# Kernel optimization log

Measured on AMD Instinct MI355X. Metric: run time of the kernel, lower is better.

Reference implementation:

```python
import jax, jax.numpy as jnp
import numpy as np

HIDDEN = 256


def setup_inputs() -> dict:
    key = jax.random.key(0)
    ks = jax.random.split(key, 16)
    bs, T, wv, vocab, inp = 256, 256, 100, 600, 64
    s = 0.05
    lengths = jax.random.randint(ks[2], (bs,), 2, T + 1)
    lengths = lengths.at[0].set(T)  # ensure max(decoder_length) == T-1
    return {
        "encoder_out": jax.random.normal(ks[0], (bs, inp), jnp.float32),
        "encoded_captions": jax.random.normal(ks[1], (bs, T, wv), jnp.float32),
        "w_ih": jax.random.normal(ks[3], (4 * HIDDEN, inp), jnp.float32) * s,
        "w_hh": jax.random.normal(ks[4], (4 * HIDDEN, HIDDEN), jnp.float32) * s,
        "b_ih": jax.random.normal(ks[5], (4 * HIDDEN,), jnp.float32) * s,
        "b_hh": jax.random.normal(ks[6], (4 * HIDDEN,), jnp.float32) * s,
        "W_out": jax.random.normal(ks[7], (vocab, HIDDEN), jnp.float32) * s,
        "b_out": jax.random.normal(ks[8], (vocab,), jnp.float32) * s,
        "W_emb": jax.random.normal(ks[9], (inp, wv), jnp.float32) * s,
        "b_emb": jax.random.normal(ks[10], (inp,), jnp.float32) * s,
        "W_h": jax.random.normal(ks[11], (HIDDEN, inp), jnp.float32) * s,
        "b_h": jax.random.normal(ks[12], (HIDDEN,), jnp.float32) * s,
        "W_c": jax.random.normal(ks[13], (HIDDEN, inp), jnp.float32) * s,
        "b_c": jax.random.normal(ks[14], (HIDDEN,), jnp.float32) * s,
        "caption_lengths": lengths,
    }


def reference(encoder_out, encoded_captions, w_ih, w_hh, b_ih, b_hh,
              W_out, b_out, W_emb, b_emb, W_h, b_h, W_c, b_c,
              caption_lengths):
    # sort by descending caption length (as torch.sort(descending=True))
    sort_idx = jnp.argsort(-caption_lengths)
    lengths = caption_lengths[sort_idx]
    enc = encoder_out[sort_idx]                  # [bs, 64]
    caps = encoded_captions[sort_idx]            # [bs, T, 100]

    h0 = enc @ W_h.T + b_h                       # [bs, H]
    c0 = enc @ W_c.T + b_c                       # [bs, H]
    emb = caps @ W_emb.T + b_emb                 # [bs, T, 64]

    dec_len = lengths - 1                        # [bs]
    steps = caps.shape[1] - 1                    # == max(dec_len) by construction
    xs = jnp.swapaxes(emb[:, :steps], 0, 1)      # [steps, bs, 64]
    ts = jnp.arange(steps)

    def step(carry, inp):
        h, c = carry
        x, t = inp
        gates = x @ w_ih.T + b_ih + h @ w_hh.T + b_hh      # [bs, 4H]
        i, f, g, o = jnp.split(gates, 4, axis=-1)           # torch gate order i,f,g,o
        i = jax.nn.sigmoid(i); f = jax.nn.sigmoid(f)
        g = jnp.tanh(g);       o = jax.nn.sigmoid(o)
        c_new = f * c + i * g
        h_new = o * jnp.tanh(c_new)
        active = (t < dec_len)[:, None]                     # shrinking batch == mask (sorted)
        logits = h_new @ W_out.T + b_out                    # [bs, vocab]
        pred = jnp.where(active, logits, jnp.float32(-1.0))
        h = jnp.where(active, h_new, h)
        c = jnp.where(active, c_new, c)
        return (h, c), pred

    (_, _), preds = jax.lax.scan(step, (h0, c0), (xs, ts))
    predicts = jnp.swapaxes(preds, 0, 1)         # [bs, steps, vocab]
    return predicts, caps, dec_len, sort_idx
```

## Files before the change

### kernel.cpp

```cpp
#include <hip/hip_runtime.h>
#include <hip/hip_fp16.h>

#define BS 256
#define T 256
#define STEPS 255
#define WV 100
#define INP 64
#define H 256
#define G4 1024
#define VOCAB 600
#define VT 38

typedef _Float16 f16x2 __attribute__((ext_vector_type(2)));
typedef _Float16 f16x8 __attribute__((ext_vector_type(8)));
typedef float f32x4 __attribute__((ext_vector_type(4)));

__device__ __forceinline__ float fdot2(unsigned w, unsigned h, float acc) {
#if defined(__has_builtin) && __has_builtin(__builtin_amdgcn_fdot2)
    return __builtin_amdgcn_fdot2(__builtin_bit_cast(f16x2, w),
                                  __builtin_bit_cast(f16x2, h), acc, false);
#else
    __half2 wv = *(const __half2*)&w;
    __half2 hv = *(const __half2*)&h;
    float2 wf = __half22float2(wv), hf = __half22float2(hv);
    return acc + wf.x * hf.x + wf.y * hf.y;
#endif
}

__device__ __forceinline__ float quad_reduce(float x) {
    int a = __builtin_bit_cast(int, x);
    int b = __builtin_amdgcn_update_dpp(0, a, 0xB1, 0xF, 0xF, true);
    float s = x + __builtin_bit_cast(float, b);
    int c = __builtin_bit_cast(int, s);
    int d = __builtin_amdgcn_update_dpp(0, c, 0x4E, 0xF, 0xF, true);
    return s + __builtin_bit_cast(float, d);
}

__device__ __forceinline__ f32x4 mfma16(uint4 a, uint4 b, f32x4 c) {
    return __builtin_amdgcn_mfma_f32_16x16x32_f16(
        __builtin_bit_cast(f16x8, a), __builtin_bit_cast(f16x8, b), c, 0, 0, 0);
}

__global__ void k_sort(const int* __restrict__ lens, int* __restrict__ sidx,
                       int* __restrict__ dlen, float* __restrict__ out_dec,
                       float* __restrict__ out_sidx) {
    __shared__ int L[BS];
    int i = threadIdx.x;
    L[i] = lens[i];
    __syncthreads();
    int li = L[i];
    int r = 0;
    for (int j = 0; j < BS; ++j) {
        int lj = L[j];
        r += (lj > li) || (lj == li && j < i);
    }
    sidx[r] = i;
    dlen[r] = li - 1;
    out_sidx[r] = (float)i;
    out_dec[r]  = (float)(li - 1);
}

__global__ void k_gather(const float* __restrict__ cin, const int* __restrict__ sidx,
                         float* __restrict__ cout) {
    int b = blockIdx.x;
    int src = sidx[b];
    const float4* in  = (const float4*)(cin + (size_t)src * T * WV);
    float4* out       = (float4*)(cout + (size_t)b * T * WV);
    for (int i = threadIdx.x; i < T * WV / 4; i += 256) out[i] = in[i];
}

__global__ void k_wcomb(const float* __restrict__ w_ih, const float* __restrict__ W_emb,
                        float* __restrict__ Wc) {
    int idx = blockIdx.x * 256 + threadIdx.x;
    int r = idx / WV, cc = idx % WV;
    float acc = 0.f;
    for (int k = 0; k < INP; ++k) acc += w_ih[r * INP + k] * W_emb[k * WV + cc];
    Wc[idx] = acc;
}

__global__ void k_bcomb(const float* __restrict__ w_ih, const float* __restrict__ b_ih,
                        const float* __restrict__ b_hh, const float* __restrict__ b_emb,
                        float* __restrict__ bc) {
    int r = blockIdx.x * 256 + threadIdx.x;
    float acc = b_ih[r] + b_hh[r];
    for (int k = 0; k < INP; ++k) acc += w_ih[r * INP + k] * b_emb[k];
    bc[r] = acc;
}

__global__ void k_packw(const float* __restrict__ w_hh, __half2* __restrict__ wR) {
    int idx = blockIdx.x * 256 + threadIdx.x;
    wR[idx] = __floats2half2_rn(w_hh[(size_t)idx * 2], w_hh[(size_t)idx * 2 + 1]);
}

__global__ void k_packwo(const float* __restrict__ Wo, __half* __restrict__ woHi,
                         __half* __restrict__ woLo) {
    int idx = blockIdx.x * 256 + threadIdx.x;
    int fi = idx >> 9;
    int l  = (idx >> 3) & 63;
    int j  = idx & 7;
    int vt = fi >> 3, kt = fi & 7;
    int v = vt * 16 + (l & 15);
    int k = kt * 32 + ((l >> 4) << 3) + j;
    float w = (v < VOCAB) ? Wo[(size_t)v * H + k] : 0.f;
    __half hi = __float2half(w);
    __half lo = __float2half(w - __half2float(hi));
    woHi[idx] = hi;
    woLo[idx] = lo;
}

__global__ void k_inithc(const float* __restrict__ enc, const int* __restrict__ sidx,
                         const float* __restrict__ W_h, const float* __restrict__ b_h,
                         const float* __restrict__ W_c, const float* __restrict__ b_c,
                         float* __restrict__ h_st, float* __restrict__ c_st) {
    int b = blockIdx.x, j = threadIdx.x;
    __shared__ __align__(16) float e[INP];
    int src = sidx[b];
    if (j < INP) e[j] = enc[src * INP + j];
    __syncthreads();
    const float4* e4  = (const float4*)e;
    const float4* wh4 = (const float4*)(W_h + (size_t)j * INP);
    const float4* wc4 = (const float4*)(W_c + (size_t)j * INP);
    float ah = b_h[j], ac = b_c[j];
    #pragma unroll
    for (int k4 = 0; k4 < INP / 4; ++k4) {
        float4 ev = e4[k4];
        float4 wh = wh4[k4];
        float4 wc = wc4[k4];
        ah += ev.x * wh.x + ev.y * wh.y + ev.z * wh.z + ev.w * wh.w;
        ac += ev.x * wc.x + ev.y * wc.y + ev.z * wc.z + ev.w * wc.w;
    }
    h_st[b * H + j] = ah;
    c_st[b * H + j] = ac;
}

__global__ void k_xg(const float* __restrict__ caps, const float* __restrict__ Wc,
                     const float* __restrict__ bc, const int* __restrict__ dlen,
                     float* __restrict__ xg, int t0, int Cc) {
    int b = blockIdx.y;
    int ct0 = blockIdx.x * 16;
    if (t0 + ct0 >= dlen[b]) return;
    __shared__ __align__(16) float4 cs4[16][WV / 4];
    float* cs = (float*)cs4;
    for (int i = threadIdx.x; i < 16 * WV; i += 256) {
        int rr = i / WV, k = i % WV;
        int t = t0 + ct0 + rr;
        cs[rr * WV + k] = (t < T && ct0 + rr < Cc) ? caps[((size_t)b * T + t) * WV + k] : 0.f;
    }
    __syncthreads();
    int nrow = Cc - ct0; if (nrow > 16) nrow = 16;
    for (int rq = 0; rq < 4; ++rq) {
        int r = threadIdx.x + rq * 256;
        float acc[16];
        float bv = bc[r];
        #pragma unroll
        for (int rr = 0; rr < 16; ++rr) acc[rr] = bv;
        const float4* wr = (const float4*)(Wc + (size_t)r * WV);
        for (int k4 = 0; k4 < WV / 4; ++k4) {
            float4 w = wr[k4];
            #pragma unroll
            for (int rr = 0; rr < 16; ++rr) {
                float4 av = cs4[rr][k4];
                acc[rr] += av.x * w.x + av.y * w.y + av.z * w.z + av.w * w.w;
            }
        }
        for (int rr = 0; rr < nrow; ++rr)
            xg[((size_t)b * Cc + ct0 + rr) * G4 + r] = acc[rr];
    }
}

#define LSTM_SMEM (131072 + 4096 + 1152)

__global__ __launch_bounds__(512)
__attribute__((amdgpu_waves_per_eu(2, 2)))
void k_lstm(const __half2* __restrict__ wR,
        const float* __restrict__ xg, const int* __restrict__ dlen,
        float* __restrict__ h_st, float* __restrict__ c_st,
        __half* __restrict__ hck, int t0, int Cc) {
    extern __shared__ __align__(16) char smem[];
    uint4*    wl4  = (uint4*)smem;
    float*    gv   = (float*)(smem + 131072);
    unsigned* hpad = (unsigned*)(smem + 131072 + 4096);
    unsigned* lpad = hpad + 144;
    const uint4* hh4 = (const uint4*)hpad;
    const uint4* hl4 = (const uint4*)lpad;

    int b = blockIdx.x, tid = threadIdx.x;
    int steps_b = dlen[b];
    if (t0 >= steps_b) return;

    int lane = tid & 63;
    int q = lane & 3;
    int Q = tid >> 2;
    int rowbase = Q * 8;
    int gate = __builtin_amdgcn_readfirstlane(tid >> 7);

    const uint4* wR4 = (const uint4*)wR;

    uint4 wreg[6][8];
    #pragma unroll
    for (int j = 0; j < 6; ++j)
        #pragma unroll
        for (int u = 0; u < 8; ++u)
            wreg[j][u] = wR4[(rowbase + j) * 32 + q * 8 + u];
    #pragma unroll
    for (int s = 0; s < 2; ++s)
        #pragma unroll
        for (int u = 0; u < 8; ++u)
            wl4[((u * 2 + s) * 128 + Q) * 4 + q] = wR4[(rowbase + 6 + s) * 32 + q * 8 + u];

    float c = 0.f, hcur = 0.f;
    if (tid < H) {
        hcur = h_st[b * H + tid];
        c    = c_st[b * H + tid];
        __half hh16 = __float2half(hcur);
        __half hl16 = __float2half(hcur - __half2float(hh16));
        int hidx = (tid >> 6) * 72 + (tid & 63);
        ((__half*)hpad)[hidx] = hh16;
        ((__half*)lpad)[hidx] = hl16;
    }
    __syncthreads();

    int tend = t0 + Cc; if (tend > steps_b) tend = steps_b;
    const float* xgp = xg + (size_t)b * Cc * G4;
    __half* hckp = hck + (size_t)b * Cc * H;

    for (int t = t0; t < tend; ++t) {
        float x0 = xgp[rowbase + q];
        float x1 = xgp[rowbase + 4 + q];

        float ah[8], al[8];
        #pragma unroll
        for (int j = 0; j < 8; ++j) { ah[j] = 0.f; al[j] = 0.f; }

        #pragma unroll
        for (int u = 0; u < 8; ++u) {
            uint4 hh = hh4[q * 9 + u];
            uint4 hl = hl4[q * 9 + u];
            #pragma unroll
            for (int j = 0; j < 6; ++j) {
                uint4 w = wreg[j][u];
                ah[j] = fdot2(w.x, hh.x, ah[j]);
                ah[j] = fdot2(w.y, hh.y, ah[j]);
                ah[j] = fdot2(w.z, hh.z, ah[j]);
                ah[j] = fdot2(w.w, hh.w, ah[j]);
                al[j] = fdot2(w.x, hl.x, al[j]);
                al[j] = fdot2(w.y, hl.y, al[j]);
                al[j] = fdot2(w.z, hl.z, al[j]);
                al[j] = fdot2(w.w, hl.w, al[j]);
            }
            uint4 w6 = wl4[((u * 2 + 0) * 128 + Q) * 4 + q];
            uint4 w7 = wl4[((u * 2 + 1) * 128 + Q) * 4 + q];
            ah[6] = fdot2(w6.x, hh.x, ah[6]);
            ah[6] = fdot2(w6.y, hh.y, ah[6]);
            ah[6] = fdot2(w6.z, hh.z, ah[6]);
            ah[6] = fdot2(w6.w, hh.w, ah[6]);
            al[6] = fdot2(w6.x, hl.x, al[6]);
            al[6] = fdot2(w6.y, hl.y, al[6]);
            al[6] = fdot2(w6.z, hl.z, al[6]);
            al[6] = fdot2(w6.w, hl.w, al[6]);
            ah[7] = fdot2(w7.x, hh.x, ah[7]);
            ah[7] = fdot2(w7.y, hh.y, ah[7]);
            ah[7] = fdot2(w7.z, hh.z, ah[7]);
            ah[7] = fdot2(w7.w, hh.w, ah[7]);
            al[7] = fdot2(w7.x, hl.x, al[7]);
            al[7] = fdot2(w7.y, hl.y, al[7]);
            al[7] = fdot2(w7.z, hl.z, al[7]);
            al[7] = fdot2(w7.w, hl.w, al[7]);
        }

        float tt[8];
        #pragma unroll
        for (int j = 0; j < 8; ++j) tt[j] = quad_reduce(ah[j] + al[j]);

        float k0 = (q == 0) ? tt[0] : (q == 1) ? tt[1] : (q == 2) ? tt[2] : tt[3];
        float k1 = (q == 0) ? tt[4] : (q == 1) ? tt[5] : (q == 2) ? tt[6] : tt[7];
        float p0 = k0 + x0;
        float p1 = k1 + x1;
        if (gate == 2) { p0 = tanhf(p0); p1 = tanhf(p1); }
        else {
            p0 = 1.f / (1.f + __expf(-p0));
            p1 = 1.f / (1.f + __expf(-p1));
        }
        gv[rowbase + q]     = p0;
        gv[rowbase + 4 + q] = p1;
        __syncthreads();

        if (tid < H) {
            float iv  = gv[tid];
            float fv  = gv[256 + tid];
            float gvt = gv[512 + tid];
            float ov  = gv[768 + tid];
            c = fv * c + iv * gvt;
            float nh = ov * tanhf(c);
            hcur = nh;
            __half hh16 = __float2half(nh);
            __half hl16 = __float2half(nh - __half2float(hh16));
            hckp[tid] = hh16;
            int hidx = (tid >> 6) * 72 + (tid & 63);
            ((__half*)hpad)[hidx] = hh16;
            ((__half*)lpad)[hidx] = hl16;
        }
        __syncthreads();
        xgp += G4;
        hckp += H;
    }
    if (tid < H) { h_st[b * H + tid] = hcur; c_st[b * H + tid] = c; }
}

__global__ __launch_bounds__(64) void k_logits(const __half* __restrict__ hck,
        const __half* __restrict__ woHi, const __half* __restrict__ woLo,
        const float* __restrict__ bo, const int* __restrict__ dlen,
        float* __restrict__ pred, int t0, int Cc) {
    int b = blockIdx.y;
    int ct0 = blockIdx.x * 32;
    if (ct0 >= Cc) return;
    int steps_b = dlen[b];
    int l = threadIdx.x;
    int lhi = l >> 4, llo = l & 15;

    if (t0 + ct0 >= steps_b) {
        for (int r = 0; r < 32; ++r) {
            int t = t0 + ct0 + r;
            if (r >= Cc - ct0 || t >= STEPS) break;
            float* pr = pred + ((size_t)b * STEPS + t) * VOCAB;
            for (int v = l; v < VOCAB; v += 64) pr[v] = -1.f;
        }
        return;
    }

    uint4 a[2][8];
    #pragma unroll
    for (int m = 0; m < 2; ++m) {
        int rr = ct0 + m * 16 + llo;
        int rc = (rr < Cc) ? rr : (Cc - 1);
        const uint4* rp = (const uint4*)(hck + ((size_t)b * Cc + rc) * H);
        #pragma unroll
        for (int kt = 0; kt < 8; ++kt) a[m][kt] = rp[kt * 4 + lhi];
    }

    const uint4* bh4 = (const uint4*)woHi;
    const uint4* bl4 = (const uint4*)woLo;
    for (int vt = 0; vt < VT; ++vt) {
        int v = vt * 16 + llo;
        float bias = (v < VOCAB) ? bo[v] : 0.f;
        f32x4 acc0 = {bias, bias, bias, bias};
        f32x4 acc1 = acc0;
        #pragma unroll
        for (int kt = 0; kt < 8; ++kt) {
            uint4 bh = bh4[(vt * 8 + kt) * 64 + l];
            acc0 = mfma16(a[0][kt], bh, acc0);
            acc1 = mfma16(a[1][kt], bh, acc1);
        }
        #pragma unroll
        for (int kt = 0; kt < 8; ++kt) {
            uint4 bl = bl4[(vt * 8 + kt) * 64 + l];
            acc0 = mfma16(a[0][kt], bl, acc0);
            acc1 = mfma16(a[1][kt], bl, acc1);
        }
        if (v < VOCAB) {
            #pragma unroll
            for (int m = 0; m < 2; ++m) {
                f32x4 A = m ? acc1 : acc0;
                #pragma unroll
                for (int i = 0; i < 4; ++i) {
                    int r = ct0 + m * 16 + lhi * 4 + i;
                    int t = t0 + r;
                    if (r < Cc && t < STEPS)
                        pred[((size_t)b * STEPS + t) * VOCAB + v] =
                            (t < steps_b) ? A[i] : -1.f;
                }
            }
        }
    }
}

extern "C" void kernel_launch(void* const* d_in, const int* in_sizes, int n_in,
                              void* d_out, int out_size, void* d_ws, size_t ws_size,
                              hipStream_t stream) {
    const float* enc   = (const float*)d_in[0];
    const float* caps  = (const float*)d_in[1];
    const float* w_ih  = (const float*)d_in[2];
    const float* w_hh  = (const float*)d_in[3];
    const float* b_ih  = (const float*)d_in[4];
    const float* b_hh  = (const float*)d_in[5];
    const float* W_out = (const float*)d_in[6];
    const float* b_out = (const float*)d_in[7];
    const float* W_emb = (const float*)d_in[8];
    const float* b_emb = (const float*)d_in[9];
    const float* W_h   = (const float*)d_in[10];
    const float* b_h   = (const float*)d_in[11];
    const float* W_c   = (const float*)d_in[12];
    const float* b_c   = (const float*)d_in[13];
    const int*   lens  = (const int*)d_in[14];

    float* out_pred = (float*)d_out;
    float* out_caps = out_pred + (size_t)BS * STEPS * VOCAB;
    float* out_dec  = out_caps + (size_t)BS * T * WV;
    float* out_sidx = out_dec + BS;

    char* w = (char*)d_ws;
    size_t off = 0;
    auto take = [&](size_t bytes) -> char* {
        char* p = w + off;
        off += (bytes + 255) & ~(size_t)255;
        return p;
    };
    int*     sidx = (int*)take(BS * 4);
    int*     dlen = (int*)take(BS * 4);
    float*   Wc   = (float*)take((size_t)G4 * WV * 4);
    float*   bc   = (float*)take(G4 * 4);
    float*   h_st = (float*)take((size_t)BS * H * 4);
    float*   c_st = (float*)take((size_t)BS * H * 4);
    __half2* wR   = (__half2*)take((size_t)G4 * (H / 2) * 4);
    __half*  woHi = (__half*)take((size_t)VT * 8 * 64 * 8 * 2);
    __half*  woLo = (__half*)take((size_t)VT * 8 * 64 * 8 * 2);

    size_t rem = (ws_size > off) ? (ws_size - off) : 0;
    size_t per_step = (size_t)BS * G4 * 4 + (size_t)BS * H * 2 + 1024;
    int C = (int)(rem / per_step);
    if (C < 1) C = 1;
    if (C > STEPS) C = STEPS;
    float*  xg  = (float*)take((size_t)BS * C * G4 * 4);
    __half* hck = (__half*)take((size_t)BS * C * H * 2);

    (void)hipFuncSetAttribute((const void*)k_lstm,
                              hipFuncAttributeMaxDynamicSharedMemorySize, LSTM_SMEM);

    k_sort<<<1, 256, 0, stream>>>(lens, sidx, dlen, out_dec, out_sidx);
    k_gather<<<BS, 256, 0, stream>>>(caps, sidx, out_caps);
    k_wcomb<<<G4 * WV / 256, 256, 0, stream>>>(w_ih, W_emb, Wc);
    k_bcomb<<<G4 / 256, 256, 0, stream>>>(w_ih, b_ih, b_hh, b_emb, bc);
    k_packw<<<G4 * (H / 2) / 256, 256, 0, stream>>>(w_hh, wR);
    k_packwo<<<VT * 8 * 64 * 8 / 256, 256, 0, stream>>>(W_out, woHi, woLo);
    k_inithc<<<BS, 256, 0, stream>>>(enc, sidx, W_h, b_h, W_c, b_c, h_st, c_st);

    for (int t0 = 0; t0 < STEPS; t0 += C) {
        int Cc = STEPS - t0; if (Cc > C) Cc = C;
        dim3 gx((Cc + 15) / 16, BS);
        dim3 gl((Cc + 31) / 32, BS);
        k_xg<<<gx, 256, 0, stream>>>(out_caps, Wc, bc, dlen, xg, t0, Cc);
        k_lstm<<<BS, 512, LSTM_SMEM, stream>>>(wR, xg, dlen, h_st, c_st, hck, t0, Cc);
        k_logits<<<gl, 64, 0, stream>>>(hck, woHi, woLo, b_out, dlen, out_pred, t0, Cc);
    }
}
```

Measured before the change: 1.504 ms.

## Compute input-gate projection with split-fp16 MFMA instead of scalar FP32

Caption embeddings and the combined input weight are each split into fp16 hi/lo pairs and packed into MFMA fragment layouts. The xg kernel then uses 16x16 MFMA tiles with three products per tile (hi*hi, hi*lo, lo*hi) in place of the FP32 scalar dot-product loop. This targets the FP32 ALU cost of the input projection. It adds two pack kernels and extra workspace for the packed captions, and slightly changes numerics.

```diff
diff --git a/kernel.cpp b/kernel.cpp
--- a/kernel.cpp
+++ b/kernel.cpp
@@ -106,6 +106,32 @@
     __half lo = __float2half(w - __half2float(hi));
     woHi[idx] = hi;
     woLo[idx] = lo;
+}
+
+__global__ void k_packcaps(const float* __restrict__ caps, __half* __restrict__ cHi,
+                           __half* __restrict__ cLo) {
+    int idx = blockIdx.x * 256 + threadIdx.x;
+    int k = idx & 127;
+    int bt = idx >> 7;
+    float v = (k < WV) ? caps[(size_t)bt * WV + k] : 0.f;
+    __half hi = __float2half(v);
+    cHi[idx] = hi;
+    cLo[idx] = __float2half(v - __half2float(hi));
+}
+
+__global__ void k_packwc(const float* __restrict__ Wc, __half* __restrict__ wcHi,
+                         __half* __restrict__ wcLo) {
+    int idx = blockIdx.x * 256 + threadIdx.x;
+    int fi = idx >> 9;
+    int l  = (idx >> 3) & 63;
+    int j  = idx & 7;
+    int nt = fi >> 2, kt = fi & 3;
+    int n = nt * 16 + (l & 15);
+    int k = kt * 32 + ((l >> 4) << 3) + j;
+    float w = (k < WV) ? Wc[(size_t)n * WV + k] : 0.f;
+    __half hi = __float2half(w);
+    wcHi[idx] = hi;
+    wcLo[idx] = __float2half(w - __half2float(hi));
 }
 
 __global__ void k_inithc(const float* __restrict__ enc, const int* __restrict__ sidx,
@@ -133,38 +159,57 @@
     c_st[b * H + j] = ac;
 }
 
-__global__ void k_xg(const float* __restrict__ caps, const float* __restrict__ Wc,
-                     const float* __restrict__ bc, const int* __restrict__ dlen,
-                     float* __restrict__ xg, int t0, int Cc) {
+__global__ __launch_bounds__(256) void k_xg(const __half* __restrict__ cHi,
+        const __half* __restrict__ cLo, const __half* __restrict__ wcHi,
+        const __half* __restrict__ wcLo, const float* __restrict__ bc,
+        const int* __restrict__ dlen, float* __restrict__ xg, int t0, int Cc) {
     int b = blockIdx.y;
-    int ct0 = blockIdx.x * 16;
+    int ct0 = blockIdx.x * 32;
     if (t0 + ct0 >= dlen[b]) return;
-    __shared__ __align__(16) float4 cs4[16][WV / 4];
-    float* cs = (float*)cs4;
-    for (int i = threadIdx.x; i < 16 * WV; i += 256) {
-        int rr = i / WV, k = i % WV;
-        int t = t0 + ct0 + rr;
-        cs[rr * WV + k] = (t < T && ct0 + rr < Cc) ? caps[((size_t)b * T + t) * WV + k] : 0.f;
-    }
-    __syncthreads();
-    int nrow = Cc - ct0; if (nrow > 16) nrow = 16;
-    for (int rq = 0; rq < 4; ++rq) {
-        int r = threadIdx.x + rq * 256;
-        float acc[16];
-        float bv = bc[r];
-        #pragma unroll
-        for (int rr = 0; rr < 16; ++rr) acc[rr] = bv;
-        const float4* wr = (const float4*)(Wc + (size_t)r * WV);
-        for (int k4 = 0; k4 < WV / 4; ++k4) {
-            float4 w = wr[k4];
+    int tid = threadIdx.x;
+    int l = tid & 63, wid = tid >> 6;
+    int lhi = l >> 4, llo = l & 15;
+
+    uint4 aH[2][4], aL[2][4];
+    #pragma unroll
+    for (int m = 0; m < 2; ++m) {
+        int rr = ct0 + m * 16 + llo;
+        if (rr >= Cc) rr = Cc - 1;
+        size_t base = ((size_t)b * T + (t0 + rr)) * 128 + lhi * 8;
+        #pragma unroll
+        for (int kt = 0; kt < 4; ++kt) {
+            aH[m][kt] = *(const uint4*)(cHi + base + kt * 32);
+            aL[m][kt] = *(const uint4*)(cLo + base + kt * 32);
+        }
+    }
+    const uint4* bh4 = (const uint4*)wcHi;
+    const uint4* bl4 = (const uint4*)wcLo;
+    for (int i = 0; i < 16; ++i) {
+        int nt = wid * 16 + i;
+        float bias = bc[nt * 16 + llo];
+        f32x4 acc0 = {bias, bias, bias, bias};
+        f32x4 acc1 = acc0;
+        #pragma unroll
+        for (int kt = 0; kt < 4; ++kt) {
+            uint4 bh = bh4[(nt * 4 + kt) * 64 + l];
+            uint4 bl = bl4[(nt * 4 + kt) * 64 + l];
+            acc0 = mfma16(aH[0][kt], bh, acc0);
+            acc1 = mfma16(aH[1][kt], bh, acc1);
+            acc0 = mfma16(aH[0][kt], bl, acc0);
+            acc1 = mfma16(aH[1][kt], bl, acc1);
+            acc0 = mfma16(aL[0][kt], bh, acc0);
+            acc1 = mfma16(aL[1][kt], bh, acc1);
+        }
+        #pragma unroll
+        for (int m = 0; m < 2; ++m) {
+            f32x4 A = m ? acc1 : acc0;
             #pragma unroll
-            for (int rr = 0; rr < 16; ++rr) {
-                float4 av = cs4[rr][k4];
-                acc[rr] += av.x * w.x + av.y * w.y + av.z * w.z + av.w * w.w;
+            for (int ii = 0; ii < 4; ++ii) {
+                int rr = ct0 + m * 16 + lhi * 4 + ii;
+                if (rr < Cc)
+                    xg[((size_t)b * Cc + rr) * G4 + nt * 16 + llo] = A[ii];
             }
         }
-        for (int rr = 0; rr < nrow; ++rr)
-            xg[((size_t)b * Cc + ct0 + rr) * G4 + r] = acc[rr];
     }
 }
 
@@ -414,6 +459,10 @@
     __half2* wR   = (__half2*)take((size_t)G4 * (H / 2) * 4);
     __half*  woHi = (__half*)take((size_t)VT * 8 * 64 * 8 * 2);
     __half*  woLo = (__half*)take((size_t)VT * 8 * 64 * 8 * 2);
+    __half*  cHi  = (__half*)take((size_t)BS * T * 128 * 2);
+    __half*  cLo  = (__half*)take((size_t)BS * T * 128 * 2);
+    __half*  wcHi = (__half*)take((size_t)64 * 4 * 64 * 8 * 2);
+    __half*  wcLo = (__half*)take((size_t)64 * 4 * 64 * 8 * 2);
 
     size_t rem = (ws_size > off) ? (ws_size - off) : 0;
     size_t per_step = (size_t)BS * G4 * 4 + (size_t)BS * H * 2 + 1024;
@@ -432,14 +481,15 @@
     k_bcomb<<<G4 / 256, 256, 0, stream>>>(w_ih, b_ih, b_hh, b_emb, bc);
     k_packw<<<G4 * (H / 2) / 256, 256, 0, stream>>>(w_hh, wR);
     k_packwo<<<VT * 8 * 64 * 8 / 256, 256, 0, stream>>>(W_out, woHi, woLo);
+    k_packcaps<<<BS * T * 128 / 256, 256, 0, stream>>>(out_caps, cHi, cLo);
+    k_packwc<<<64 * 4 * 64 * 8 / 256, 256, 0, stream>>>(Wc, wcHi, wcLo);
     k_inithc<<<BS, 256, 0, stream>>>(enc, sidx, W_h, b_h, W_c, b_c, h_st, c_st);
 
     for (int t0 = 0; t0 < STEPS; t0 += C) {
         int Cc = STEPS - t0; if (Cc > C) Cc = C;
-        dim3 gx((Cc + 15) / 16, BS);
-        dim3 gl((Cc + 31) / 32, BS);
-        k_xg<<<gx, 256, 0, stream>>>(out_caps, Wc, bc, dlen, xg, t0, Cc);
+        dim3 gx((Cc + 31) / 32, BS);
+        k_xg<<<gx, 256, 0, stream>>>(cHi, cLo, wcHi, wcLo, bc, dlen, xg, t0, Cc);
         k_lstm<<<BS, 512, LSTM_SMEM, stream>>>(wR, xg, dlen, h_st, c_st, hck, t0, Cc);
-        k_logits<<<gl, 64, 0, stream>>>(hck, woHi, woLo, b_out, dlen, out_pred, t0, Cc);
-    }
-}
+        k_logits<<<gx, 64, 0, stream>>>(hck, woHi, woLo, b_out, dlen, out_pred, t0, Cc);
+    }
+}
```

New measurement: 1.320 ms. -12.2%, faster.
